# Kernel tuning notes

Hardware: AMD Instinct MI355X
Metric: run time of the kernel (lower is better)

The kernel has to match this reference:

```python
import jax, jax.numpy as jnp
import numpy as np
import math

# Static multi-level spatial layout (H, W) per level and flattened start offsets.
SHAPES = ((100, 100), (50, 50), (25, 25), (13, 13))
STARTS = (0, 10000, 12500, 13125)
LEN_IN = 13294
D_MODEL, N_LEVELS, N_HEADS, N_POINTS = 256, 4, 8, 4
D_HEAD = D_MODEL // N_HEADS
B, LQ = 2, 13294


def _offset_bias():
    # Replicates MSDeformAttn._reset_parameters radial grid init for sampling_offsets.bias
    thetas = np.arange(N_HEADS, dtype=np.float32) * (2.0 * math.pi / N_HEADS)
    grid = np.stack([np.cos(thetas), np.sin(thetas)], axis=-1)  # [nh, 2]
    grid = grid / np.abs(grid).max(axis=-1, keepdims=True)
    # [nh, nl, np, 2] with per-point radius (i+1)
    full = np.tile(grid[:, None, None, :], (1, N_LEVELS, N_POINTS, 1))
    full = full * np.arange(1, N_POINTS + 1, dtype=np.float32)[None, None, :, None]
    return full.reshape(-1)


def setup_inputs() -> dict:
    key = jax.random.key(0)
    ks = jax.random.split(key, 8)
    xavier = 1.0 / math.sqrt(D_MODEL)
    return {
        "query": jax.random.normal(ks[0], (B, LQ, D_MODEL), jnp.float32),
        "reference_points": jax.random.uniform(ks[1], (B, LQ, N_LEVELS, 2), jnp.float32),
        "input_flatten": jax.random.normal(ks[2], (B, LEN_IN, D_MODEL), jnp.float32),
        "input_spatial_shapes": jnp.array(SHAPES, jnp.int32),
        "input_level_start_index": jnp.array(STARTS, jnp.int32),
        "W_off": jax.random.normal(ks[3], (D_MODEL, N_HEADS * N_LEVELS * N_POINTS * 2), jnp.float32) * 0.01,
        "b_off": jnp.asarray(_offset_bias()),
        "W_attn": jax.random.normal(ks[4], (D_MODEL, N_HEADS * N_LEVELS * N_POINTS), jnp.float32) * 0.02,
        "b_attn": jnp.zeros((N_HEADS * N_LEVELS * N_POINTS,), jnp.float32),
        "W_val": jax.random.normal(ks[5], (D_MODEL, D_MODEL), jnp.float32) * xavier,
        "b_val": jnp.zeros((D_MODEL,), jnp.float32),
        "W_out": jax.random.normal(ks[6], (D_MODEL, D_MODEL), jnp.float32) * xavier,
        "b_out": jnp.zeros((D_MODEL,), jnp.float32),
    }


def reference(query, reference_points, input_flatten, input_spatial_shapes,
              input_level_start_index, W_off, b_off, W_attn, b_attn,
              W_val, b_val, W_out, b_out):
    Bq, Lq, _ = query.shape
    value = (input_flatten @ W_val + b_val).reshape(Bq, LEN_IN, N_HEADS, D_HEAD)

    off = (query @ W_off + b_off).reshape(Bq, Lq, N_HEADS, N_LEVELS, N_POINTS, 2)
    aw = (query @ W_attn + b_attn).reshape(Bq, Lq, N_HEADS, N_LEVELS * N_POINTS)
    aw = jax.nn.softmax(aw, axis=-1).reshape(Bq, Lq, N_HEADS, N_LEVELS, N_POINTS)

    # offset normalizer is (W, H) per level
    normalizer = jnp.array([[w, h] for (h, w) in SHAPES], query.dtype)  # [nl, 2]
    loc = reference_points[:, :, None, :, None, :] + off / normalizer[None, None, None, :, None, :]

    bi = jnp.arange(Bq)[:, None, None, None]
    hi = jnp.arange(N_HEADS)[None, None, :, None]
    out = jnp.zeros((Bq, Lq, N_HEADS, D_HEAD), query.dtype)

    # Per-level zero-padded bilinear sampling (math-equivalent to grid_sample
    # align_corners=False, padding_mode='zeros' on the padded max_H x max_W grid,
    # since the padded region is zero-filled).
    for lvl, (H, W) in enumerate(SHAPES):
        s = STARTS[lvl]
        vflat = value[:, s:s + H * W]  # [B, H*W, nh, dh]
        l = loc[:, :, :, lvl]          # [B, Lq, nh, P, 2] in normalized coords
        x = l[..., 0] * W - 0.5
        y = l[..., 1] * H - 0.5
        x0 = jnp.floor(x)
        y0 = jnp.floor(y)
        sampled = jnp.zeros((Bq, Lq, N_HEADS, N_POINTS, D_HEAD), query.dtype)
        for dx in (0, 1):
            for dy in (0, 1):
                xi = x0 + dx
                yi = y0 + dy
                wgt = (1.0 - jnp.abs(x - xi)) * (1.0 - jnp.abs(y - yi))
                valid = (xi >= 0) & (xi <= W - 1) & (yi >= 0) & (yi <= H - 1)
                idx = (jnp.clip(yi, 0, H - 1) * W + jnp.clip(xi, 0, W - 1)).astype(jnp.int32)
                v = vflat[bi, idx, hi]  # [B, Lq, nh, P, dh]
                sampled = sampled + v * (wgt * valid)[..., None]
        out = out + jnp.einsum('bqhpd,bqhp->bqhd', sampled, aw[:, :, :, lvl])

    out = out.reshape(Bq, Lq, D_MODEL)
    return out @ W_out + b_out
```

## Files before the change

kernel.cpp:

```cpp
#include <hip/hip_runtime.h>
#include <math.h>

#define BQ 2
#define LQ 13294
#define LEN_IN 13294
#define M_ROWS 26588

__device__ __constant__ int c_HW[4]    = {100, 50, 25, 13};
__device__ __constant__ int c_START[4] = {0, 10000, 12500, 13125};

typedef __attribute__((ext_vector_type(8))) short bf16x8;
typedef __attribute__((ext_vector_type(4))) float f32x4;

__device__ inline unsigned short f2bf(float f) {
  union { float f; unsigned int u; } x; x.f = f;
  unsigned int u = x.u;
  return (unsigned short)((u + 0x7fffu + ((u >> 16) & 1u)) >> 16);
}
__device__ inline float h2f(unsigned short h) {
  _Float16 x; __builtin_memcpy(&x, &h, 2); return (float)x;
}
__device__ inline unsigned short f2h(float f) {
  _Float16 x = (_Float16)f; unsigned short u; __builtin_memcpy(&u, &x, 2); return u;
}

__device__ inline void gl_lds16(const void* g, void* l) {
  __builtin_amdgcn_global_load_lds(
      (const __attribute__((address_space(1))) unsigned int*)g,
      (__attribute__((address_space(3))) unsigned int*)l, 16, 0, 0);
}

#define CONV_BLKS 3456
#define N4EACH (M_ROWS * 64)

__global__ __launch_bounds__(256) void prep_all(
    const float* __restrict__ query, const float* __restrict__ inpf,
    const float* __restrict__ W_off, const float* __restrict__ b_off,
    const float* __restrict__ W_attn, const float* __restrict__ b_attn,
    const float* __restrict__ W_val, const float* __restrict__ W_out,
    unsigned short* __restrict__ q_bf, unsigned short* __restrict__ in_bf,
    unsigned short* __restrict__ Wval_t, unsigned short* __restrict__ Woa_t,
    unsigned short* __restrict__ Wout_t, float* __restrict__ b_oa) {
  const int bx = blockIdx.x;
  if (bx < CONV_BLKS) {
    int i = bx * 256 + threadIdx.x;
    const int stride = CONV_BLKS * 256;
    for (; i < 2 * N4EACH; i += stride) {
      const float* src; unsigned short* dst; int j;
      if (i < N4EACH) { src = query; dst = q_bf; j = i; }
      else            { src = inpf;  dst = in_bf; j = i - N4EACH; }
      const float4 v = ((const float4*)src)[j];
      ushort4 h;
      h.x = f2bf(v.x); h.y = f2bf(v.y); h.z = f2bf(v.z); h.w = f2bf(v.w);
      ((ushort4*)dst)[j] = h;
    }
    return;
  }
  const int idx = (bx - CONV_BLKS) * 256 + threadIdx.x;
  const int SZ1 = 256 * 256;
  const int SZ2 = 384 * 256;
  if (idx < SZ1) {
    const int n = idx >> 8, k = idx & 255;
    Wval_t[idx] = f2bf(W_val[k * 256 + n]);
  } else if (idx < SZ1 + SZ2) {
    const int j = idx - SZ1;
    const int n = j >> 8, k = j & 255;
    const float v = (n < 256) ? W_off[k * 256 + n] : W_attn[k * 128 + (n - 256)];
    Woa_t[j] = f2bf(v);
  } else {
    const int j = idx - SZ1 - SZ2;
    const int n = j >> 8, k = j & 255;
    Wout_t[j] = f2bf(W_out[k * 256 + n]);
  }
  if (bx == CONV_BLKS) b_oa[threadIdx.x] = b_off[threadIdx.x];
  if (bx == CONV_BLKS + 1 && threadIdx.x < 128)
    b_oa[256 + threadIdx.x] = b_attn[threadIdx.x];
}

template <int CT>
__device__ inline void gemm_body(
    const unsigned short* __restrict__ A, const unsigned short* __restrict__ Wt,
    const float* __restrict__ bias, void* __restrict__ Cp,
    int M, int N, int m0, int n0,
    unsigned short* As, unsigned short* Bs) {
  const int tid = threadIdx.x;
  const int wv = tid >> 6;
  const int lane = tid & 63;
  const int wm = (wv & 1) * 64;
  const int wn = (wv >> 1) * 64;
  const int fr = lane & 15;
  const int fq = lane >> 4;
  const int lr = lane >> 3;
  const int gch = (lane & 7) ^ lr;

  const unsigned short* ga[4];
  const unsigned short* gb[4];
#pragma unroll
  for (int t = 0; t < 4; ++t) {
    int ar = m0 + wv * 32 + t * 8 + lr;
    if (ar > M - 1) ar = M - 1;
    ga[t] = A + (size_t)ar * 256 + gch * 8;
    gb[t] = Wt + (size_t)(n0 + wv * 32 + t * 8 + lr) * 256 + gch * 8;
  }

  f32x4 acc[4][4];
#pragma unroll
  for (int i = 0; i < 4; ++i)
#pragma unroll
    for (int j = 0; j < 4; ++j) acc[i][j] = (f32x4){0.f, 0.f, 0.f, 0.f};

  for (int k0 = 0; k0 < 256; k0 += 64) {
    __syncthreads();
#pragma unroll
    for (int t = 0; t < 4; ++t) {
      gl_lds16(ga[t], &As[(wv * 32 + t * 8) * 64]);
      gl_lds16(gb[t], &Bs[(wv * 32 + t * 8) * 64]);
      ga[t] += 64; gb[t] += 64;
    }
    __syncthreads();
#pragma unroll
    for (int kk = 0; kk < 2; ++kk) {
      bf16x8 af[4], bf[4];
#pragma unroll
      for (int i = 0; i < 4; ++i) {
        const int row = wm + i * 16 + fr;
        af[i] = *(const bf16x8*)&As[row * 64 + ((kk * 4 + fq) ^ (row & 7)) * 8];
      }
#pragma unroll
      for (int j = 0; j < 4; ++j) {
        const int row = wn + j * 16 + fr;
        bf[j] = *(const bf16x8*)&Bs[row * 64 + ((kk * 4 + fq) ^ (row & 7)) * 8];
      }
#pragma unroll
      for (int i = 0; i < 4; ++i)
#pragma unroll
        for (int j = 0; j < 4; ++j)
          acc[i][j] = __builtin_amdgcn_mfma_f32_16x16x32_bf16(bf[j], af[i],
                                                              acc[i][j], 0, 0, 0);
    }
  }

#pragma unroll
  for (int j = 0; j < 4; ++j) {
    const int nb = n0 + wn + j * 16 + fq * 4;
    const float4 b4 = *(const float4*)&bias[nb];
#pragma unroll
    for (int i = 0; i < 4; ++i) {
      const int m = m0 + wm + i * 16 + fr;
      if (m >= M) continue;
      const float v0 = acc[i][j][0] + b4.x;
      const float v1 = acc[i][j][1] + b4.y;
      const float v2 = acc[i][j][2] + b4.z;
      const float v3 = acc[i][j][3] + b4.w;
      if (CT == 0) {
        float4 o = make_float4(v0, v1, v2, v3);
        *(float4*)&((float*)Cp)[(size_t)m * N + nb] = o;
      } else if (CT == 1) {
        uint2 o;
        o.x = (unsigned int)f2bf(v0) | ((unsigned int)f2bf(v1) << 16);
        o.y = (unsigned int)f2bf(v2) | ((unsigned int)f2bf(v3) << 16);
        *(uint2*)&((unsigned short*)Cp)[(size_t)m * N + nb] = o;
      } else {
        uint2 o;
        o.x = (unsigned int)f2h(v0) | ((unsigned int)f2h(v1) << 16);
        o.y = (unsigned int)f2h(v2) | ((unsigned int)f2h(v3) << 16);
        *(uint2*)&((unsigned short*)Cp)[(size_t)m * N + nb] = o;
      }
    }
  }
}

__global__ __launch_bounds__(256) void gemm_fused(
    const unsigned short* __restrict__ in_bf,
    const unsigned short* __restrict__ q_bf,
    const unsigned short* __restrict__ Wval_t,
    const unsigned short* __restrict__ Woa_t,
    const float* __restrict__ b_val, const float* __restrict__ b_oa,
    void* __restrict__ v_buf, void* __restrict__ oa_buf) {
  __shared__ unsigned short As[128 * 64];
  __shared__ unsigned short Bs[128 * 64];
  const int m0 = blockIdx.x * 128;
  if (blockIdx.y < 2) {
    gemm_body<1>(in_bf, Wval_t, b_val, v_buf, M_ROWS, 256,
                 m0, blockIdx.y * 128, As, Bs);
  } else {
    gemm_body<2>(q_bf, Woa_t, b_oa, oa_buf, M_ROWS, 384,
                 m0, (blockIdx.y - 2) * 128, As, Bs);
  }
}

__global__ __launch_bounds__(256) void gemm_out(
    const unsigned short* __restrict__ mid,
    const unsigned short* __restrict__ Wout_t,
    const float* __restrict__ b_out, float* __restrict__ out) {
  __shared__ unsigned short As[128 * 64];
  __shared__ unsigned short Bs[128 * 64];
  gemm_body<0>(mid, Wout_t, b_out, out, M_ROWS, 256,
               blockIdx.x * 128, blockIdx.y * 128, As, Bs);
}

__global__ __launch_bounds__(256) void sample_kernel(
    const float* __restrict__ refp,
    const unsigned short* __restrict__ oa,
    const unsigned short* __restrict__ value,
    unsigned int* __restrict__ mid) {
  const int tid = threadIdx.x;
  const int qi = tid >> 7;
  const int q = blockIdx.x * 2 + qi;
  const int b = (q >= LQ) ? 1 : 0;

  __shared__ float2 s_wo[2][4][136];

  {
    const int pid = tid & 127;
    const int h = pid >> 4;
    const int lp = pid & 15;
    const int l = lp >> 2;
    const int p = lp & 3;
    const int HW = c_HW[l];
    const float fW = (float)HW;

    const float logit = h2f(oa[(size_t)q * 384 + 256 + pid]);
    float mx = logit;
#pragma unroll
    for (int s = 1; s < 16; s <<= 1) mx = fmaxf(mx, __shfl_xor(mx, s, 16));
    const float e = expf(logit - mx);
    float sum = e;
#pragma unroll
    for (int s = 1; s < 16; s <<= 1) sum += __shfl_xor(sum, s, 16);
    const float a = e / sum;

    const unsigned int opk =
        *(const unsigned int*)&oa[(size_t)q * 384 + h * 32 + l * 8 + p * 2];
    const float ox = h2f((unsigned short)(opk & 0xffffu));
    const float oy = h2f((unsigned short)(opk >> 16));
    const float rx = refp[((size_t)q * 4 + l) * 2 + 0];
    const float ry = refp[((size_t)q * 4 + l) * 2 + 1];
    const float x = (rx + ox / fW) * fW - 0.5f;
    const float y = (ry + oy / fW) * fW - 0.5f;
    const float x0 = floorf(x);
    const float y0 = floorf(y);

#pragma unroll
    for (int t = 0; t < 4; ++t) {
      const int dx = t & 1;
      const int dy = t >> 1;
      const float xi = x0 + (float)dx;
      const float yi = y0 + (float)dy;
      const float wgt = (1.0f - fabsf(x - xi)) * (1.0f - fabsf(y - yi));
      const bool valid =
          (xi >= 0.f) && (xi <= fW - 1.f) && (yi >= 0.f) && (yi <= fW - 1.f);
      int xc = (int)xi; xc = xc < 0 ? 0 : (xc > HW - 1 ? HW - 1 : xc);
      int yc = (int)yi; yc = yc < 0 ? 0 : (yc > HW - 1 ? HW - 1 : yc);
      const int row = b * LEN_IN + c_START[l] + yc * HW + xc;
      float2 wo;
      wo.x = valid ? wgt * a : 0.f;
      wo.y = __int_as_float(row * 512 + h * 64);
      s_wo[qi][t][h * 17 + lp] = wo;
    }
  }
  __syncthreads();

  {
    const int g = tid & 127;
    const int h = g >> 4;
    const int dp = g & 15;
    const char* vbase = (const char*)value + dp * 4;
    float acc0 = 0.f, acc1 = 0.f;
#pragma unroll 4
    for (int lp = 0; lp < 16; ++lp) {
      const int si = h * 17 + lp;
#pragma unroll
      for (int t = 0; t < 4; ++t) {
        const float2 f = s_wo[qi][t][si];
        const unsigned int v = *(const unsigned int*)(vbase + __float_as_int(f.y));
        acc0 += f.x * __uint_as_float(v << 16);
        acc1 += f.x * __uint_as_float(v & 0xffff0000u);
      }
    }
    mid[(size_t)q * 128 + h * 16 + dp] =
        (unsigned int)f2bf(acc0) | ((unsigned int)f2bf(acc1) << 16);
  }
}

extern "C" void kernel_launch(void* const* d_in, const int* in_sizes, int n_in,
                              void* d_out, int out_size, void* d_ws,
                              size_t ws_size, hipStream_t stream) {
  const float* query  = (const float*)d_in[0];
  const float* refp   = (const float*)d_in[1];
  const float* inpf   = (const float*)d_in[2];
  const float* W_off  = (const float*)d_in[5];
  const float* b_off  = (const float*)d_in[6];
  const float* W_attn = (const float*)d_in[7];
  const float* b_attn = (const float*)d_in[8];
  const float* W_val  = (const float*)d_in[9];
  const float* b_val  = (const float*)d_in[10];
  const float* W_out  = (const float*)d_in[11];
  const float* b_out  = (const float*)d_in[12];
  float* out = (float*)d_out;

  unsigned char* w = (unsigned char*)d_ws;
  unsigned short* Wval_t = (unsigned short*)w;  w += 256 * 256 * 2;
  unsigned short* Woa_t  = (unsigned short*)w;  w += 384 * 256 * 2;
  unsigned short* Wout_t = (unsigned short*)w;  w += 256 * 256 * 2;
  float*          b_oa   = (float*)w;           w += 384 * 4 + 64;
  unsigned short* q_bf   = (unsigned short*)w;  w += (size_t)M_ROWS * 256 * 2;
  unsigned short* in_bf  = (unsigned short*)w;  w += (size_t)M_ROWS * 256 * 2;
  unsigned short* v_buf  = (unsigned short*)w;  w += (size_t)M_ROWS * 256 * 2;
  unsigned short* oa_buf = (unsigned short*)w;  w += (size_t)M_ROWS * 384 * 2;
  unsigned int*   mid_buf = (unsigned int*)w;

  const dim3 blk(256);
  const int mg = (M_ROWS + 127) / 128;

  prep_all<<<dim3(CONV_BLKS + 896), blk, 0, stream>>>(
      query, inpf, W_off, b_off, W_attn, b_attn, W_val, W_out,
      q_bf, in_bf, Wval_t, Woa_t, Wout_t, b_oa);
  gemm_fused<<<dim3(mg, 5), blk, 0, stream>>>(in_bf, q_bf, Wval_t, Woa_t,
                                              b_val, b_oa, v_buf, oa_buf);
  sample_kernel<<<dim3(M_ROWS / 2), blk, 0, stream>>>(refp, oa_buf, v_buf,
                                                      mid_buf);
  gemm_out<<<dim3(mg, 2), blk, 0, stream>>>((const unsigned short*)mid_buf,
                                            Wout_t, b_out, out);
}
```

Baseline: 214.2 us.

## Stage full-K weight tile in LDS and stream A fragments from global

Replaces the K-looped LDS-staged GEMM with a variant that loads the entire 128x256 weight slice into LDS once, then has each wave read its A rows straight from global memory into registers while iterating over all of K. This removes the per-K-step barriers and the A staging through LDS, and changes the wave tiling from 64x64 to 32x128 per wave. The LDS footprint grows to 64KB per block, which may reduce occupancy. The A loads are uncoalesced 16-byte reads with no prefetch overlap.

```diff
diff --git a/kernel.cpp b/kernel.cpp
--- a/kernel.cpp
+++ b/kernel.cpp
@@ -78,83 +78,66 @@
 }
 
 template <int CT>
-__device__ inline void gemm_body(
+__device__ inline void gemm_stream(
     const unsigned short* __restrict__ A, const unsigned short* __restrict__ Wt,
     const float* __restrict__ bias, void* __restrict__ Cp,
-    int M, int N, int m0, int n0,
-    unsigned short* As, unsigned short* Bs) {
+    int M, int N, int m0, int n0, unsigned short* Ws) {
   const int tid = threadIdx.x;
   const int wv = tid >> 6;
   const int lane = tid & 63;
-  const int wm = (wv & 1) * 64;
-  const int wn = (wv >> 1) * 64;
   const int fr = lane & 15;
   const int fq = lane >> 4;
-  const int lr = lane >> 3;
-  const int gch = (lane & 7) ^ lr;
-
-  const unsigned short* ga[4];
-  const unsigned short* gb[4];
-#pragma unroll
-  for (int t = 0; t < 4; ++t) {
-    int ar = m0 + wv * 32 + t * 8 + lr;
-    if (ar > M - 1) ar = M - 1;
-    ga[t] = A + (size_t)ar * 256 + gch * 8;
-    gb[t] = Wt + (size_t)(n0 + wv * 32 + t * 8 + lr) * 256 + gch * 8;
-  }
-
-  f32x4 acc[4][4];
-#pragma unroll
-  for (int i = 0; i < 4; ++i)
-#pragma unroll
-    for (int j = 0; j < 4; ++j) acc[i][j] = (f32x4){0.f, 0.f, 0.f, 0.f};
-
-  for (int k0 = 0; k0 < 256; k0 += 64) {
-    __syncthreads();
-#pragma unroll
-    for (int t = 0; t < 4; ++t) {
-      gl_lds16(ga[t], &As[(wv * 32 + t * 8) * 64]);
-      gl_lds16(gb[t], &Bs[(wv * 32 + t * 8) * 64]);
-      ga[t] += 64; gb[t] += 64;
-    }
-    __syncthreads();
-#pragma unroll
-    for (int kk = 0; kk < 2; ++kk) {
-      bf16x8 af[4], bf[4];
-#pragma unroll
-      for (int i = 0; i < 4; ++i) {
-        const int row = wm + i * 16 + fr;
-        af[i] = *(const bf16x8*)&As[row * 64 + ((kk * 4 + fq) ^ (row & 7)) * 8];
-      }
-#pragma unroll
-      for (int j = 0; j < 4; ++j) {
-        const int row = wn + j * 16 + fr;
-        bf[j] = *(const bf16x8*)&Bs[row * 64 + ((kk * 4 + fq) ^ (row & 7)) * 8];
-      }
-#pragma unroll
-      for (int i = 0; i < 4; ++i)
-#pragma unroll
-        for (int j = 0; j < 4; ++j)
-          acc[i][j] = __builtin_amdgcn_mfma_f32_16x16x32_bf16(bf[j], af[i],
-                                                              acc[i][j], 0, 0, 0);
-    }
-  }
-
-#pragma unroll
-  for (int j = 0; j < 4; ++j) {
-    const int nb = n0 + wn + j * 16 + fq * 4;
+
+#pragma unroll
+  for (int it = 0; it < 16; ++it) {
+    const int lin = wv * 1024 + it * 64 + lane;
+    const int r = lin >> 5;
+    const int p = lin & 31;
+    const int c = p ^ (r & 7);
+    gl_lds16(Wt + (size_t)(n0 + r) * 256 + c * 8,
+             &Ws[(size_t)(wv * 1024 + it * 64) * 8]);
+  }
+  __syncthreads();
+
+  int mr0 = m0 + wv * 32 + fr;       if (mr0 > M - 1) mr0 = M - 1;
+  int mr1 = m0 + wv * 32 + 16 + fr;  if (mr1 > M - 1) mr1 = M - 1;
+  const unsigned short* a0 = A + (size_t)mr0 * 256 + fq * 8;
+  const unsigned short* a1 = A + (size_t)mr1 * 256 + fq * 8;
+
+  f32x4 acc[2][8];
+#pragma unroll
+  for (int mt = 0; mt < 2; ++mt)
+#pragma unroll
+    for (int n = 0; n < 8; ++n) acc[mt][n] = (f32x4){0.f, 0.f, 0.f, 0.f};
+
+#pragma unroll
+  for (int kk = 0; kk < 8; ++kk) {
+    const bf16x8 af0 = *(const bf16x8*)(a0 + kk * 32);
+    const bf16x8 af1 = *(const bf16x8*)(a1 + kk * 32);
+#pragma unroll
+    for (int n = 0; n < 8; ++n) {
+      const int rn = n * 16 + fr;
+      const bf16x8 b =
+          *(const bf16x8*)&Ws[rn * 256 + (((kk * 4 + fq) ^ (rn & 7)) * 8)];
+      acc[0][n] = __builtin_amdgcn_mfma_f32_16x16x32_bf16(b, af0, acc[0][n], 0, 0, 0);
+      acc[1][n] = __builtin_amdgcn_mfma_f32_16x16x32_bf16(b, af1, acc[1][n], 0, 0, 0);
+    }
+  }
+
+#pragma unroll
+  for (int n = 0; n < 8; ++n) {
+    const int nb = n0 + n * 16 + fq * 4;
     const float4 b4 = *(const float4*)&bias[nb];
 #pragma unroll
-    for (int i = 0; i < 4; ++i) {
-      const int m = m0 + wm + i * 16 + fr;
+    for (int mt = 0; mt < 2; ++mt) {
+      const int m = m0 + wv * 32 + mt * 16 + fr;
       if (m >= M) continue;
-      const float v0 = acc[i][j][0] + b4.x;
-      const float v1 = acc[i][j][1] + b4.y;
-      const float v2 = acc[i][j][2] + b4.z;
-      const float v3 = acc[i][j][3] + b4.w;
+      const float v0 = acc[mt][n][0] + b4.x;
+      const float v1 = acc[mt][n][1] + b4.y;
+      const float v2 = acc[mt][n][2] + b4.z;
+      const float v3 = acc[mt][n][3] + b4.w;
       if (CT == 0) {
-        float4 o = make_float4(v0, v1, v2, v3);
-        *(float4*)&((float*)Cp)[(size_t)m * N + nb] = o;
+        *(float4*)&((float*)Cp)[(size_t)m * N + nb] = make_float4(v0, v1, v2, v3);
       } else if (CT == 1) {
         uint2 o;
         o.x = (unsigned int)f2bf(v0) | ((unsigned int)f2bf(v1) << 16);
@@ -170,22 +153,21 @@
   }
 }
 
-__global__ __launch_bounds__(256) void gemm_fused(
+__global__ __launch_bounds__(256) void gemm_vo(
     const unsigned short* __restrict__ in_bf,
     const unsigned short* __restrict__ q_bf,
     const unsigned short* __restrict__ Wval_t,
     const unsigned short* __restrict__ Woa_t,
     const float* __restrict__ b_val, const float* __restrict__ b_oa,
     void* __restrict__ v_buf, void* __restrict__ oa_buf) {
-  __shared__ unsigned short As[128 * 64];
-  __shared__ unsigned short Bs[128 * 64];
+  __shared__ unsigned short Ws[128 * 256];
   const int m0 = blockIdx.x * 128;
   if (blockIdx.y < 2) {
-    gemm_body<1>(in_bf, Wval_t, b_val, v_buf, M_ROWS, 256,
-                 m0, blockIdx.y * 128, As, Bs);
+    gemm_stream<1>(in_bf, Wval_t, b_val, v_buf, M_ROWS, 256,
+                   m0, blockIdx.y * 128, Ws);
   } else {
-    gemm_body<2>(q_bf, Woa_t, b_oa, oa_buf, M_ROWS, 384,
-                 m0, (blockIdx.y - 2) * 128, As, Bs);
+    gemm_stream<2>(q_bf, Woa_t, b_oa, oa_buf, M_ROWS, 384,
+                   m0, (blockIdx.y - 2) * 128, Ws);
   }
 }
 
@@ -193,10 +175,9 @@
     const unsigned short* __restrict__ mid,
     const unsigned short* __restrict__ Wout_t,
     const float* __restrict__ b_out, float* __restrict__ out) {
-  __shared__ unsigned short As[128 * 64];
-  __shared__ unsigned short Bs[128 * 64];
-  gemm_body<0>(mid, Wout_t, b_out, out, M_ROWS, 256,
-               blockIdx.x * 128, blockIdx.y * 128, As, Bs);
+  __shared__ unsigned short Ws[128 * 256];
+  gemm_stream<0>(mid, Wout_t, b_out, out, M_ROWS, 256,
+                 blockIdx.x * 128, blockIdx.y * 128, Ws);
 }
 
 __global__ __launch_bounds__(256) void sample_kernel(
@@ -316,8 +297,8 @@
   prep_all<<<dim3(CONV_BLKS + 896), blk, 0, stream>>>(
       query, inpf, W_off, b_off, W_attn, b_attn, W_val, W_out,
       q_bf, in_bf, Wval_t, Woa_t, Wout_t, b_oa);
-  gemm_fused<<<dim3(mg, 5), blk, 0, stream>>>(in_bf, q_bf, Wval_t, Woa_t,
-                                              b_val, b_oa, v_buf, oa_buf);
+  gemm_vo<<<dim3(mg, 5), blk, 0, stream>>>(in_bf, q_bf, Wval_t, Woa_t,
+                                           b_val, b_oa, v_buf, oa_buf);
   sample_kernel<<<dim3(M_ROWS / 2), blk, 0, stream>>>(refp, oa_buf, v_buf,
                                                       mid_buf);
   gemm_out<<<dim3(mg, 2), blk, 0, stream>>>((const unsigned short*)mid_buf,
```

Result: no change. 212.6 us (-0.7%).
